# Kernel tuning notes

Measured on AMD Instinct MI355X. Metric: run time of the kernel, lower is better.

Reference implementation:

```python
import jax, jax.numpy as jnp
import numpy as np

SOS = 1  # from init_kwargs

def gru_cell(x, h, W_ih, W_hh, b_ih, b_hh):
    # torch nn.GRU single-step cell semantics
    gi = x @ W_ih.T + b_ih            # [B, 3H]
    gh = h @ W_hh.T + b_hh            # [B, 3H]
    i_r, i_z, i_n = jnp.split(gi, 3, axis=-1)
    h_r, h_z, h_n = jnp.split(gh, 3, axis=-1)
    r = jax.nn.sigmoid(i_r + h_r)
    z = jax.nn.sigmoid(i_z + h_z)
    n = jnp.tanh(i_n + r * h_n)
    return (1.0 - z) * n + z * h

def setup_inputs() -> dict:
    key = jax.random.key(0)
    ks = jax.random.split(key, 12)
    V, E, H, L, B = 32000, 512, 512, 2, 32
    s = lambda k, shape: (jax.random.normal(k, shape, jnp.float32) * 0.05)
    return dict(
        h_0=s(ks[0], (L, B, H)),
        emb=s(ks[1], (V, E)),
        W_ih0=s(ks[2], (3 * H, E)), W_hh0=s(ks[3], (3 * H, H)),
        b_ih0=s(ks[4], (3 * H,)),   b_hh0=s(ks[5], (3 * H,)),
        W_ih1=s(ks[6], (3 * H, H)), W_hh1=s(ks[7], (3 * H, H)),
        b_ih1=s(ks[8], (3 * H,)),   b_hh1=s(ks[9], (3 * H,)),
        W_out=s(ks[10], (V, H)),    b_out=s(ks[11], (V,)),
        max_n=64,
    )

def reference(h_0, emb, W_ih0, W_hh0, b_ih0, b_hh0,
              W_ih1, W_hh1, b_ih1, b_hh1, W_out, b_out, max_n):
    B = h_0.shape[1]
    tok0 = jnp.full((B,), SOS, dtype=jnp.int32)

    def step(carry, _):
        h, tok = carry                              # h: [2, B, H], tok: [B]
        x = emb[tok]                                # [B, E] embedding gather
        h0n = gru_cell(x,   h[0], W_ih0, W_hh0, b_ih0, b_hh0)
        h1n = gru_cell(h0n, h[1], W_ih1, W_hh1, b_ih1, b_hh1)
        logits = h1n @ W_out.T + b_out              # [B, V]
        ntok = jnp.argmax(logits, axis=-1).astype(jnp.int32)
        return (jnp.stack([h0n, h1n]), ntok), ntok

    (h_t, _), toks = jax.lax.scan(step, (h_0, tok0), None, length=max_n)
    # toks: [max_n, B] -> [B, max_n] to mirror per-sequence output lists
    return toks.T, h_t
```

## Files before the change

### kernel.cpp

```cpp
#include <hip/hip_runtime.h>
#include <math.h>

#define NBLK 256
#define NTHR 512
#define Bsz  32
#define Hsz  512
#define Vsz  32000
#define BH   (Bsz*Hsz)
#define LDP  516
#define CBLK 250
#define EPS  0.0045f

#define WS_HBUF   0
#define WS_PACKED 131072
#define WS_PLB    135168
#define WS_BAR    139264
#define WS_WPACK  143360
#define WS_WNORM  32911360
#define WS_CBAR   33039360
#define WS_NEEDED 33043456

#define PACKED_SEED 0x00000000FFFFFFFEull

typedef short short8 __attribute__((ext_vector_type(8)));
typedef float f32x4  __attribute__((ext_vector_type(4)));

struct Args {
  const float* h0_init;
  const float* emb;
  const float* Wih0; const float* Whh0; const float* bih0; const float* bhh0;
  const float* Wih1; const float* Whh1; const float* bih1; const float* bhh1;
  const float* Wout; const float* bout;
  const int*   maxn;
  float* out;
  float* hbuf;
  unsigned long long* packed;
  unsigned* plb;
  unsigned* bar;
  unsigned* cbar;
  const unsigned* wpack;
  const float* wnormE;
};

__device__ __forceinline__ unsigned short bf16_rne(float f){
  unsigned u = __float_as_uint(f);
  unsigned r = u + 0x7FFFu + ((u >> 16) & 1u);
  return (unsigned short)(r >> 16);
}
__device__ __forceinline__ float bf16v(float f){
  unsigned u = ((unsigned)bf16_rne(f)) << 16;
  return __uint_as_float(u);
}
__device__ __forceinline__ unsigned short bf16_ru(float f){
  unsigned u = __float_as_uint(f);
  unsigned t = u >> 16;
  if (!(u & 0x80000000u)) { if (u & 0xFFFFu) t++; }
  return (unsigned short)t;
}
__device__ __forceinline__ unsigned key32(float f){
  unsigned u = __float_as_uint(f);
  return (u & 0x80000000u) ? ~u : (u | 0x80000000u);
}

__device__ __forceinline__ unsigned long long cload8(const void* p){
  return __hip_atomic_load((const unsigned long long*)p,
                           __ATOMIC_RELAXED, __HIP_MEMORY_SCOPE_AGENT);
}
__device__ __forceinline__ unsigned cload4u(const unsigned* p){
  return __hip_atomic_load(p, __ATOMIC_RELAXED, __HIP_MEMORY_SCOPE_AGENT);
}
__device__ __forceinline__ void cstore4(float* p, float v){
  __hip_atomic_store(p, v, __ATOMIC_RELAXED, __HIP_MEMORY_SCOPE_AGENT);
}
__device__ __forceinline__ void cstore4u(unsigned* p, unsigned v){
  __hip_atomic_store(p, v, __ATOMIC_RELAXED, __HIP_MEMORY_SCOPE_AGENT);
}
__device__ __forceinline__ void cstore8(void* p, unsigned long long v){
  __hip_atomic_store((unsigned long long*)p, v,
                     __ATOMIC_RELAXED, __HIP_MEMORY_SCOPE_AGENT);
}

__device__ __forceinline__ short8 ntload8(const void* p){
  return __builtin_nontemporal_load((const short8*)p);
}

__device__ __forceinline__ void gridbar(unsigned* bar, int bid){
  __syncthreads();
  if (threadIdx.x == 0){
    asm volatile("s_waitcnt vmcnt(0)" ::: "memory");
    const int g = bid & 7;
    unsigned* gcnt = bar + g*32;
    unsigned* root = bar + 8*32;
    unsigned* gen  = bar + (9+g)*32;
    unsigned mygen = __hip_atomic_load(gen, __ATOMIC_RELAXED, __HIP_MEMORY_SCOPE_AGENT);
    unsigned go = __hip_atomic_fetch_add(gcnt, 1u, __ATOMIC_RELAXED, __HIP_MEMORY_SCOPE_AGENT);
    if (go == 31u){
      unsigned ro = __hip_atomic_fetch_add(root, 1u, __ATOMIC_RELAXED, __HIP_MEMORY_SCOPE_AGENT);
      if (ro == 7u){
        #pragma unroll
        for (int i = 0; i < 8; ++i)
          __hip_atomic_store(bar + i*32, 0u, __ATOMIC_RELAXED, __HIP_MEMORY_SCOPE_AGENT);
        __hip_atomic_store(root, 0u, __ATOMIC_RELAXED, __HIP_MEMORY_SCOPE_AGENT);
        asm volatile("s_waitcnt vmcnt(0)" ::: "memory");
        #pragma unroll
        for (int i = 0; i < 8; ++i)
          __hip_atomic_fetch_add(bar + (9+i)*32, 1u, __ATOMIC_RELAXED, __HIP_MEMORY_SCOPE_AGENT);
      }
    }
    while (__hip_atomic_load(gen, __ATOMIC_RELAXED, __HIP_MEMORY_SCOPE_AGENT) == mygen){
      __builtin_amdgcn_s_sleep(1);
    }
  }
  __syncthreads();
}

__device__ __forceinline__ void cluster_sync(unsigned* cnt, unsigned target){
  __syncthreads();
  if (threadIdx.x == 0){
    asm volatile("s_waitcnt vmcnt(0)" ::: "memory");
    __hip_atomic_fetch_add(cnt, 1u, __ATOMIC_RELAXED, __HIP_MEMORY_SCOPE_AGENT);
    while (__hip_atomic_load(cnt, __ATOMIC_RELAXED, __HIP_MEMORY_SCOPE_AGENT) < target){
      __builtin_amdgcn_s_sleep(1);
    }
  }
  __syncthreads();
}

__device__ __forceinline__ void stage_h(const float* g, float* s, int tid){
  const unsigned long long* gd = (const unsigned long long*)g;
  #pragma unroll
  for (int n = 0; n < 16; ++n){
    int idx = n*512 + tid;
    int row = idx >> 8;
    int col = idx & 255;
    unsigned long long v = __hip_atomic_load(gd + idx, __ATOMIC_RELAXED,
                                             __HIP_MEMORY_SCOPE_AGENT);
    *(unsigned long long*)(s + row*LDP + col*2) = v;
  }
}

__device__ __forceinline__ void stage_row(const float* g, float* s, int tid){
  if (tid < 256){
    unsigned long long v = __hip_atomic_load((const unsigned long long*)g + tid,
                                             __ATOMIC_RELAXED, __HIP_MEMORY_SCOPE_AGENT);
    *(unsigned long long*)(s + tid*2) = v;
  }
}

__device__ __forceinline__ float red8(float v){
  v += __shfl_xor(v, 1); v += __shfl_xor(v, 2); v += __shfl_xor(v, 4);
  return v;
}
__device__ __forceinline__ float dot4acc(float4 w, float4 x, float acc){
  return fmaf(w.x,x.x, fmaf(w.y,x.y, fmaf(w.z,x.z, fmaf(w.w,x.w, acc))));
}

__device__ __forceinline__ void dot3(const float* row, const float* W, int j,
                                     int lane8, float& g0, float& g1, float& g2){
  const float* w = W + (size_t)j * Hsz;
  float a0 = 0.f, a1 = 0.f, a2 = 0.f;
  #pragma unroll 4
  for (int i = 0; i < 16; ++i){
    int k = i*32 + lane8*4;
    float4 v = *(const float4*)(row + k);
    a0 = dot4acc(*(const float4*)(w + k),            v, a0);
    a1 = dot4acc(*(const float4*)(w + 512*512 + k),  v, a1);
    a2 = dot4acc(*(const float4*)(w + 2*512*512 + k),v, a2);
  }
  g0 = red8(a0); g1 = red8(a1); g2 = red8(a2);
}

__device__ __forceinline__ void gru_oct(
    const float* xrow, const float* hrow,
    const float* Wih, const float* Whh,
    const float* bih, const float* bhh,
    int j, int lane8, float* hout_g)
{
  const float* wir = Wih + (size_t)j * Hsz;
  const float* whr = Whh + (size_t)j * Hsz;
  float ar=0.f, az=0.f, an=0.f, hr=0.f, hz=0.f, hn=0.f;
  #pragma unroll 4
  for (int i = 0; i < 16; ++i){
    int k = i*32 + lane8*4;
    float4 xv = *(const float4*)(xrow + k);
    float4 hv = *(const float4*)(hrow + k);
    ar = dot4acc(*(const float4*)(wir + k),            xv, ar);
    az = dot4acc(*(const float4*)(wir + 512*512 + k),  xv, az);
    an = dot4acc(*(const float4*)(wir + 2*512*512 + k),xv, an);
    hr = dot4acc(*(const float4*)(whr + k),            hv, hr);
    hz = dot4acc(*(const float4*)(whr + 512*512 + k),  hv, hz);
    hn = dot4acc(*(const float4*)(whr + 2*512*512 + k),hv, hn);
  }
  ar = red8(ar); az = red8(az); an = red8(an);
  hr = red8(hr); hz = red8(hz); hn = red8(hn);
  if (lane8 == 0){
    float r = 1.f/(1.f + expf(-(ar + bih[j]       + hr + bhh[j])));
    float z = 1.f/(1.f + expf(-(az + bih[Hsz+j]   + hz + bhh[Hsz+j])));
    float n = tanhf(an + bih[2*Hsz+j] + r*(hn + bhh[2*Hsz+j]));
    cstore4(hout_g, (1.f - z)*n + z*hrow[j]);
  }
}

__global__ __launch_bounds__(512) void repack_kernel(const float* __restrict__ Wout,
                                                     unsigned* __restrict__ wpack,
                                                     float* __restrict__ wnormE){
  const int rb = blockIdx.x;
  const int g = threadIdx.x >> 6;
  const int lane = threadIdx.x & 63;
  const int n = rb*128 + g*16 + (lane & 15);
  const int kq = (lane >> 4) * 8;
  float sumsq = 0.f;
  for (int c = 0; c < 16; ++c){
    const float* p = Wout + (size_t)n*512 + c*32 + kq;
    float4 f0 = *(const float4*)p;
    float4 f1 = *(const float4*)(p + 4);
    unsigned short s0 = bf16_rne(f0.x), s1 = bf16_rne(f0.y),
                   s2 = bf16_rne(f0.z), s3 = bf16_rne(f0.w),
                   s4 = bf16_rne(f1.x), s5 = bf16_rne(f1.y),
                   s6 = bf16_rne(f1.z), s7 = bf16_rne(f1.w);
    float v;
    v = __uint_as_float(((unsigned)s0)<<16); sumsq += v*v;
    v = __uint_as_float(((unsigned)s1)<<16); sumsq += v*v;
    v = __uint_as_float(((unsigned)s2)<<16); sumsq += v*v;
    v = __uint_as_float(((unsigned)s3)<<16); sumsq += v*v;
    v = __uint_as_float(((unsigned)s4)<<16); sumsq += v*v;
    v = __uint_as_float(((unsigned)s5)<<16); sumsq += v*v;
    v = __uint_as_float(((unsigned)s6)<<16); sumsq += v*v;
    v = __uint_as_float(((unsigned)s7)<<16); sumsq += v*v;
    uint4 u;
    u.x = (unsigned)s0 | ((unsigned)s1<<16);
    u.y = (unsigned)s2 | ((unsigned)s3<<16);
    u.z = (unsigned)s4 | ((unsigned)s5<<16);
    u.w = (unsigned)s6 | ((unsigned)s7<<16);
    *(uint4*)(wpack + (size_t)(((rb*8+g)*16 + c))*256 + lane*4) = u;
  }
  sumsq += __shfl_xor(sumsq, 16);
  sumsq += __shfl_xor(sumsq, 32);
  if (lane < 16) wnormE[n] = EPS * sqrtf(sumsq);
}

__global__ __launch_bounds__(NTHR, 1) void decoder_kernel(Args a){
  const int tid = threadIdx.x;
  const int bid = blockIdx.x;
  const int wave = tid >> 6;
  const int lane = tid & 63;
  const int b  = bid >> 3;
  const int s  = bid & 7;
  const int j0 = s * 64;
  const int T = a.maxn[0];
  float* h0g = a.hbuf;
  float* h1g = a.hbuf + BH;

  __shared__ float shB[Bsz*LDP];
  __shared__ float h0row[LDP];
  __shared__ unsigned af[16*64*4];
  __shared__ unsigned long long ubq8[128*8];
  __shared__ float ghA[3][64];
  __shared__ float ghB[3][64];
  __shared__ float h0own[64];
  __shared__ float h1own[64];
  __shared__ unsigned lbmaxL[32];
  __shared__ unsigned maxlbL[32];
  __shared__ float hnormL[32];
  __shared__ int sh_tok0;
  __shared__ int candCnt;
  __shared__ int candList[512];
  unsigned short* ubq16 = (unsigned short*)ubq8;

  short8 bw[16];
  float bias = 0.f, wn = 0.f;
  if (bid < CBLK){
    const unsigned* wbase = a.wpack + (size_t)((bid*8 + wave)*16)*256 + lane*4;
    #pragma unroll
    for (int c = 0; c < 16; ++c){
      bw[c] = ntload8(wbase + c*256);
      asm volatile("" : "+a"(bw[c]));
    }
    int n = bid*128 + wave*16 + (lane & 15);
    bias = a.bout[n];
    wn = a.wnormE[n];
  }

  if (tid < 64){
    h0own[tid] = a.h0_init[(size_t)b*Hsz + j0 + tid];
    h1own[tid] = a.h0_init[BH + (size_t)b*Hsz + j0 + tid];
  }
  stage_row(a.h0_init + (size_t)b*Hsz, h0row, tid);
  stage_h(a.h0_init + BH, shB, tid);
  __syncthreads();
  {
    int oct = tid >> 3, lane8 = tid & 7;
    int j = j0 + oct;
    float hr, hz, hn;  dot3(h0row, a.Whh0, j, lane8, hr, hz, hn);
    float kr, kz, kn;  dot3(shB + b*LDP, a.Whh1, j, lane8, kr, kz, kn);
    if (lane8 == 0){
      ghA[0][oct] = hr; ghA[1][oct] = hz; ghA[2][oct] = hn;
      ghB[0][oct] = kr; ghB[1][oct] = kz; ghB[2][oct] = kn;
    }
  }
  __syncthreads();

  unsigned ctarget = 0;
  for (int t = 0; t < T; ++t){
    if (tid == 0){
      int tok = 1;
      if (t > 0){
        tok = (int)(~(unsigned)(cload8(&a.packed[b*16]) & 0xffffffffULL));
        if ((unsigned)tok >= (unsigned)Vsz) tok = 1;
      }
      sh_tok0 = tok;
    }
    __syncthreads();
    {
      int oct = tid >> 3, lane8 = tid & 7;
      int j = j0 + oct;
      const float* xrow = a.emb + (size_t)sh_tok0 * Hsz;
      float ar, az, an;  dot3(xrow, a.Wih0, j, lane8, ar, az, an);
      if (lane8 == 0){
        float hr = ghA[0][oct], hz = ghA[1][oct], hn = ghA[2][oct];
        float r = 1.f/(1.f + expf(-(ar + a.bih0[j]       + hr + a.bhh0[j])));
        float z = 1.f/(1.f + expf(-(az + a.bih0[Hsz+j]   + hz + a.bhh0[Hsz+j])));
        float n = tanhf(an + a.bih0[2*Hsz+j] + r*(hn + a.bhh0[2*Hsz+j]));
        float hnew = (1.f - z)*n + z*h0own[oct];
        cstore4(h0g + (size_t)b*Hsz + j, hnew);
        h0own[oct] = hnew;
      }
    }
    ctarget += 8;
    cluster_sync(a.cbar + b*32, ctarget);

    if (s == 0 && tid == 0){
      if (t > 0){
        unsigned long long p = cload8(&a.packed[b*16]);
        int tok = (int)(~(unsigned)(p & 0xffffffffULL));
        a.out[(size_t)b*T + (t-1)] = (float)tok;
      }
      cstore8(&a.packed[b*16], PACKED_SEED);
      cstore4u(&a.plb[b*32], 0u);
    }
    stage_row(h0g + (size_t)b*Hsz, h0row, tid);
    __syncthreads();
    {
      int oct = tid >> 3, lane8 = tid & 7;
      int j = j0 + oct;
      float ar, az, an;  dot3(h0row, a.Wih1, j, lane8, ar, az, an);
      if (lane8 == 0){
        float hr = ghB[0][oct], hz = ghB[1][oct], hn = ghB[2][oct];
        float r = 1.f/(1.f + expf(-(ar + a.bih1[j]       + hr + a.bhh1[j])));
        float z = 1.f/(1.f + expf(-(az + a.bih1[Hsz+j]   + hz + a.bhh1[Hsz+j])));
        float n = tanhf(an + a.bih1[2*Hsz+j] + r*(hn + a.bhh1[2*Hsz+j]));
        float hnew = (1.f - z)*n + z*h1own[oct];
        cstore4(h1g + (size_t)b*Hsz + j, hnew);
        h1own[oct] = hnew;
      }
    }
    gridbar(a.bar, bid);

    stage_h(h1g, shB, tid);
    if (tid < 32) lbmaxL[tid] = 0u;
    if (tid == 0) candCnt = 0;
    __syncthreads();
    {
      int oct = tid >> 3, lane8 = tid & 7;
      int j = j0 + oct;
      float hr, hz, hn;  dot3(h0row, a.Whh0, j, lane8, hr, hz, hn);
      float kr, kz, kn;  dot3(shB + b*LDP, a.Whh1, j, lane8, kr, kz, kn);
      if (lane8 == 0){
        ghA[0][oct] = hr; ghA[1][oct] = hz; ghA[2][oct] = hn;
        ghB[0][oct] = kr; ghB[1][oct] = kz; ghB[2][oct] = kn;
      }
    }
    if (bid < CBLK){
      #pragma unroll
      for (int c = 0; c < 16; ++c) asm volatile("" : "+a"(bw[c]));

      if (tid < 256){
        int hb = tid >> 3, lane8 = tid & 7;
        float sq = 0.f;
        #pragma unroll
        for (int i = 0; i < 8; ++i){
          const float* p = shB + hb*LDP + i*64 + lane8*8;
          #pragma unroll
          for (int q = 0; q < 8; ++q){ float v = bf16v(p[q]); sq = fmaf(v, v, sq); }
        }
        sq = red8(sq);
        if (lane8 == 0) hnormL[hb] = sqrtf(sq);
      }

      f32x4 accs[2];
      #pragma unroll
      for (int mt = 0; mt < 2; ++mt){
        #pragma unroll
        for (int it = 0; it < 8; ++it){
          int d = it*512 + tid;
          int c = d >> 8, al = (d >> 2) & 63, dw = d & 3;
          int m = mt*16 + (al & 15);
          int k = c*32 + ((al >> 4) * 8) + dw*2;
          unsigned lo = bf16_rne(shB[m*LDP + k]);
          unsigned hi = bf16_rne(shB[m*LDP + k + 1]);
          af[d] = lo | (hi << 16);
        }
        __syncthreads();
        f32x4 acc = {0.f, 0.f, 0.f, 0.f};
        #pragma unroll
        for (int c = 0; c < 16; ++c){
          short8 av = *(short8*)&af[(c*64 + lane)*4];
          acc = __builtin_amdgcn_mfma_f32_16x16x32_bf16(av, bw[c], acc, 0, 0, 0);
        }
        accs[mt] = acc;
        __syncthreads();
      }
      {
        int n_loc = wave*16 + (lane & 15);
        int quad = lane >> 4;
        #pragma unroll
        for (int mt = 0; mt < 2; ++mt){
          unsigned long long pk = 0ULL;
          #pragma unroll
          for (int r = 0; r < 4; ++r){
            int m = mt*16 + quad*4 + r;
            float lg = accs[mt][r] + bias;
            float mg = wn * hnormL[m];
            float lb = lg - mg;
            float ub = lg + mg;
            pk |= ((unsigned long long)bf16_ru(ub)) << (16*r);
            unsigned lk = key32(lb), o;
            o = __shfl_xor(lk, 1); lk = lk > o ? lk : o;
            o = __shfl_xor(lk, 2); lk = lk > o ? lk : o;
            o = __shfl_xor(lk, 4); lk = lk > o ? lk : o;
            o = __shfl_xor(lk, 8); lk = lk > o ? lk : o;
            if ((lane & 15) == 0) atomicMax(&lbmaxL[m], lk);
          }
          ubq8[n_loc*8 + mt*4 + quad] = pk;
        }
      }
      __syncthreads();
      if (tid < 32) atomicMax(&a.plb[tid*32], lbmaxL[tid]);
      for (int u = 0; u < 8; ++u){
        int idx = u*512 + tid;
        unsigned short q = ubq16[idx];
        float uf = __uint_as_float(((unsigned)q) << 16);
        if (key32(uf) >= lbmaxL[idx & 31]){
          int pos = atomicAdd(&candCnt, 1);
          if (pos < 512) candList[pos] = idx;
        }
      }
      __syncthreads();
      if (tid < 32){
        unsigned g = cload4u(&a.plb[tid*32]);
        unsigned l = lbmaxL[tid];
        maxlbL[tid] = g > l ? g : l;
      }
      __syncthreads();
      auto rescore = [&](int cidx){
        int n_loc = cidx >> 5, rb = cidx & 31;
        unsigned short q = ubq16[cidx];
        float uf = __uint_as_float(((unsigned)q) << 16);
        if (key32(uf) < maxlbL[rb]) return;
        int n = bid*128 + n_loc;
        const float* wrow = a.Wout + (size_t)n*512 + lane*8;
        const float* hrow = shB + rb*LDP + lane*8;
        float4 w0 = *(const float4*)wrow,      w1 = *(const float4*)(wrow + 4);
        float4 x0 = *(const float4*)hrow,      x1 = *(const float4*)(hrow + 4);
        float d = dot4acc(w0, x0, 0.f);
        d = dot4acc(w1, x1, d);
        d += __shfl_xor(d, 1);  d += __shfl_xor(d, 2);  d += __shfl_xor(d, 4);
        d += __shfl_xor(d, 8);  d += __shfl_xor(d, 16); d += __shfl_xor(d, 32);
        if (lane == 0){
          float lg = d + a.bout[n];
          unsigned long long key =
              (((unsigned long long)key32(lg)) << 32) | (unsigned)(~(unsigned)n);
          atomicMax(&a.packed[rb*16], key);
        }
      };
      int nc = candCnt;
      if (nc <= 512){
        for (int ci = wave; ci < nc; ci += 8) rescore(candList[ci]);
      } else {
        for (int ci = wave; ci < 4096; ci += 8) rescore(ci);
      }
    }
    gridbar(a.bar, bid);
  }

  if (bid == 0 && tid < Bsz){
    unsigned long long p = cload8(&a.packed[tid*16]);
    int tok = (int)(~(unsigned)(p & 0xffffffffULL));
    a.out[tid*T + (T-1)] = (float)tok;
  }
  int e = bid*NTHR + tid;
  if (e < BH/2){
    unsigned long long v0 = cload8((const unsigned long long*)h0g + e);
    unsigned long long v1 = cload8((const unsigned long long*)h1g + e);
    *((unsigned long long*)(a.out + Bsz*T) + e)      = v0;
    *((unsigned long long*)(a.out + Bsz*T + BH) + e) = v1;
  }
}

__global__ __launch_bounds__(NTHR, 1) void decoder_kernel_fb(Args a){
  const int tid = threadIdx.x;
  const int bid = blockIdx.x;
  const int T = a.maxn[0];
  float* h0g = a.hbuf;
  float* h1g = a.hbuf + BH;
  __shared__ float shA[Bsz*LDP];
  __shared__ float shB[Bsz*LDP];
  __shared__ unsigned long long lbest[32*32];
  __shared__ int sh_tok[Bsz];

  for (int t = 0; t < T; ++t){
    if (t == 0) stage_h(a.h0_init, shA, tid);
    if (tid < Bsz){
      int tok;
      if (t == 0) tok = 1;
      else {
        tok = (int)(~(unsigned)(cload8(&a.packed[tid*16]) & 0xffffffffULL));
        if ((unsigned)tok >= (unsigned)Vsz) tok = 1;
      }
      sh_tok[tid] = tok;
    }
    __syncthreads();
    {
      int oct = tid >> 3, lane8 = tid & 7;
      int b = oct & 31, jj = oct >> 5;
      int j = bid*2 + jj;
      const float* xrow = a.emb + (size_t)sh_tok[b] * Hsz;
      gru_oct(xrow, shA + b*LDP, a.Wih0, a.Whh0, a.bih0, a.bhh0,
              j, lane8, h0g + b*Hsz + j);
    }
    gridbar(a.bar, bid);
    if (bid == 0 && tid < Bsz){
      if (t > 0){
        unsigned long long p = cload8(&a.packed[tid*16]);
        a.out[tid*T + (t-1)] = (float)((int)(~(unsigned)(p & 0xffffffffULL)));
      }
      cstore8(&a.packed[tid*16], PACKED_SEED);
    }
    stage_h(h0g, shA, tid);
    if (t == 0) stage_h(a.h0_init + BH, shB, tid);
    __syncthreads();
    {
      int oct = tid >> 3, lane8 = tid & 7;
      int b = oct & 31, jj = oct >> 5;
      int j = bid*2 + jj;
      gru_oct(shA + b*LDP, shB + b*LDP, a.Wih1, a.Whh1, a.bih1, a.bhh1,
              j, lane8, h1g + b*Hsz + j);
    }
    gridbar(a.bar, bid);
    stage_h(h1g, shB, tid);
    __syncthreads();
    if (bid < CBLK){
      const int quad = tid >> 2, l4 = tid & 3;
      const int rg = quad & 31, bg = quad >> 5;
      const int rowbase = bid*128 + rg*4;
      const float* wr = a.Wout + (size_t)rowbase * Hsz;
      const float* hb = shB + bg*8*LDP;
      float acc[4][8];
      #pragma unroll
      for (int s = 0; s < 4; ++s)
        #pragma unroll
        for (int j = 0; j < 8; ++j) acc[s][j] = 0.f;
      #pragma unroll 2
      for (int i = 0; i < 32; ++i){
        const int k = i*16 + l4*4;
        float4 wv[4], hv[8];
        #pragma unroll
        for (int s = 0; s < 4; ++s) wv[s] = *(const float4*)(wr + (size_t)s*Hsz + k);
        #pragma unroll
        for (int j = 0; j < 8; ++j) hv[j] = *(const float4*)(hb + j*LDP + k);
        #pragma unroll
        for (int s = 0; s < 4; ++s)
          #pragma unroll
          for (int j = 0; j < 8; ++j) acc[s][j] = dot4acc(wv[s], hv[j], acc[s][j]);
      }
      #pragma unroll
      for (int s = 0; s < 4; ++s)
        #pragma unroll
        for (int j = 0; j < 8; ++j){
          float v = acc[s][j];
          v += __shfl_xor(v, 1); v += __shfl_xor(v, 2);
          acc[s][j] = v;
        }
      if (l4 == 0){
        float4 bv = *(const float4*)(a.bout + rowbase);
        float bb[4] = {bv.x, bv.y, bv.z, bv.w};
        #pragma unroll
        for (int j = 0; j < 8; ++j){
          float best = -3.4e38f; int bi = rowbase;
          #pragma unroll
          for (int s = 0; s < 4; ++s){
            float lv = acc[s][j] + bb[s];
            if (lv > best){ best = lv; bi = rowbase + s; }
          }
          unsigned u = __float_as_uint(best);
          unsigned key = (u & 0x80000000u) ? ~u : (u | 0x80000000u);
          lbest[rg*32 + bg*8 + j] =
              ((unsigned long long)key << 32) | (unsigned)(~(unsigned)bi);
        }
      }
      __syncthreads();
      if (tid < Bsz){
        unsigned long long m = lbest[tid];
        #pragma unroll 4
        for (int r = 1; r < 32; ++r){
          unsigned long long c = lbest[r*32 + tid];
          m = (c > m) ? c : m;
        }
        atomicMax(&a.packed[tid*16], m);
      }
    }
    gridbar(a.bar, bid);
  }
  if (bid == 0 && tid < Bsz){
    unsigned long long p = cload8(&a.packed[tid*16]);
    a.out[tid*T + (T-1)] = (float)((int)(~(unsigned)(p & 0xffffffffULL)));
  }
  int e = bid*NTHR + tid;
  if (e < BH/2){
    unsigned long long v0 = cload8((const unsigned long long*)h0g + e);
    unsigned long long v1 = cload8((const unsigned long long*)h1g + e);
    *((unsigned long long*)(a.out + Bsz*T) + e)      = v0;
    *((unsigned long long*)(a.out + Bsz*T + BH) + e) = v1;
  }
}

extern "C" void kernel_launch(void* const* d_in, const int* in_sizes, int n_in,
                              void* d_out, int out_size, void* d_ws, size_t ws_size,
                              hipStream_t stream){
  Args a;
  a.h0_init = (const float*)d_in[0];
  a.emb  = (const float*)d_in[1];
  a.Wih0 = (const float*)d_in[2];
  a.Whh0 = (const float*)d_in[3];
  a.bih0 = (const float*)d_in[4];
  a.bhh0 = (const float*)d_in[5];
  a.Wih1 = (const float*)d_in[6];
  a.Whh1 = (const float*)d_in[7];
  a.bih1 = (const float*)d_in[8];
  a.bhh1 = (const float*)d_in[9];
  a.Wout = (const float*)d_in[10];
  a.bout = (const float*)d_in[11];
  a.maxn = (const int*)d_in[12];
  a.out  = (float*)d_out;
  char* wsb = (char*)d_ws;
  a.hbuf   = (float*)(wsb + WS_HBUF);
  a.packed = (unsigned long long*)(wsb + WS_PACKED);
  a.plb    = (unsigned*)(wsb + WS_PLB);
  a.bar    = (unsigned*)(wsb + WS_BAR);
  a.cbar   = (unsigned*)(wsb + WS_CBAR);
  a.wpack  = (const unsigned*)(wsb + WS_WPACK);
  a.wnormE = (const float*)(wsb + WS_WNORM);

  hipMemsetAsync(wsb + WS_PACKED, 0, 12288, stream);

  void* params[] = { &a };
  if (ws_size >= (size_t)WS_NEEDED){
    hipMemsetAsync(wsb + WS_CBAR, 0, 4096, stream);
    repack_kernel<<<CBLK, 512, 0, stream>>>(a.Wout, (unsigned*)a.wpack, (float*)a.wnormE);
    hipLaunchCooperativeKernel((void*)decoder_kernel, dim3(NBLK), dim3(NTHR),
                               params, 0, stream);
  } else {
    hipLaunchCooperativeKernel((void*)decoder_kernel_fb, dim3(NBLK), dim3(NTHR),
                               params, 0, stream);
  }
}
```

Baseline: 2.636 ms.

## Stage layer-1 hidden state directly as bf16 and feed MFMA from row layout

The full layer-1 hidden state is now staged into shared memory as bf16 instead of fp32, converted while loading. MFMA A-operands are read directly from this row-major bf16 tile, which removes the separate repack pass into a fragment buffer and two block barriers per tile. The GRU recurrence now uses a separate fp32 row for its own batch element. Candidate rescoring loads the fp32 hidden row from global memory instead of shared, so that rescore adds global traffic in exchange for lower shared-memory use and shorter staging.

```diff
diff --git a/kernel.cpp b/kernel.cpp
--- a/kernel.cpp
+++ b/kernel.cpp
@@ -8,6 +8,7 @@
 #define Vsz  32000
 #define BH   (Bsz*Hsz)
 #define LDP  516
+#define LDPB 520
 #define CBLK 250
 #define EPS  0.0045f
 
@@ -124,6 +125,21 @@
     }
   }
   __syncthreads();
+}
+
+__device__ __forceinline__ void stage_h16(const float* g, unsigned short* s16, int tid){
+  const unsigned long long* gd = (const unsigned long long*)g;
+  #pragma unroll
+  for (int n = 0; n < 16; ++n){
+    int idx = n*512 + tid;
+    int row = idx >> 8;
+    int col2 = idx & 255;
+    unsigned long long v = __hip_atomic_load(gd + idx, __ATOMIC_RELAXED,
+                                             __HIP_MEMORY_SCOPE_AGENT);
+    unsigned short b0 = bf16_rne(__uint_as_float((unsigned)v));
+    unsigned short b1 = bf16_rne(__uint_as_float((unsigned)(v >> 32)));
+    *(unsigned*)&s16[row*LDPB + col2*2] = (unsigned)b0 | ((unsigned)b1 << 16);
+  }
 }
 
 __device__ __forceinline__ void stage_h(const float* g, float* s, int tid){
@@ -251,9 +267,9 @@
   float* h0g = a.hbuf;
   float* h1g = a.hbuf + BH;
 
-  __shared__ float shB[Bsz*LDP];
+  __shared__ __align__(16) unsigned short shB16[Bsz*LDPB];
   __shared__ float h0row[LDP];
-  __shared__ unsigned af[16*64*4];
+  __shared__ float h1row[LDP];
   __shared__ unsigned long long ubq8[128*8];
   __shared__ float ghA[3][64];
   __shared__ float ghB[3][64];
@@ -286,13 +302,13 @@
     h1own[tid] = a.h0_init[BH + (size_t)b*Hsz + j0 + tid];
   }
   stage_row(a.h0_init + (size_t)b*Hsz, h0row, tid);
-  stage_h(a.h0_init + BH, shB, tid);
+  stage_row(a.h0_init + BH + (size_t)b*Hsz, h1row, tid);
   __syncthreads();
   {
     int oct = tid >> 3, lane8 = tid & 7;
     int j = j0 + oct;
     float hr, hz, hn;  dot3(h0row, a.Whh0, j, lane8, hr, hz, hn);
-    float kr, kz, kn;  dot3(shB + b*LDP, a.Whh1, j, lane8, kr, kz, kn);
+    float kr, kz, kn;  dot3(h1row, a.Whh1, j, lane8, kr, kz, kn);
     if (lane8 == 0){
       ghA[0][oct] = hr; ghA[1][oct] = hz; ghA[2][oct] = hn;
       ghB[0][oct] = kr; ghB[1][oct] = kz; ghB[2][oct] = kn;
@@ -356,7 +372,8 @@
     }
     gridbar(a.bar, bid);
 
-    stage_h(h1g, shB, tid);
+    if (bid < CBLK) stage_h16(h1g, shB16, tid);
+    stage_row(h1g + (size_t)b*Hsz, h1row, tid);
     if (tid < 32) lbmaxL[tid] = 0u;
     if (tid == 0) candCnt = 0;
     __syncthreads();
@@ -364,7 +381,7 @@
       int oct = tid >> 3, lane8 = tid & 7;
       int j = j0 + oct;
       float hr, hz, hn;  dot3(h0row, a.Whh0, j, lane8, hr, hz, hn);
-      float kr, kz, kn;  dot3(shB + b*LDP, a.Whh1, j, lane8, kr, kz, kn);
+      float kr, kz, kn;  dot3(h1row, a.Whh1, j, lane8, kr, kz, kn);
       if (lane8 == 0){
         ghA[0][oct] = hr; ghA[1][oct] = hz; ghA[2][oct] = hn;
         ghB[0][oct] = kr; ghB[1][oct] = kz; ghB[2][oct] = kn;
@@ -379,9 +396,12 @@
         float sq = 0.f;
         #pragma unroll
         for (int i = 0; i < 8; ++i){
-          const float* p = shB + hb*LDP + i*64 + lane8*8;
+          short8 sv = *(const short8*)&shB16[hb*LDPB + i*64 + lane8*8];
           #pragma unroll
-          for (int q = 0; q < 8; ++q){ float v = bf16v(p[q]); sq = fmaf(v, v, sq); }
+          for (int q = 0; q < 8; ++q){
+            float v = __uint_as_float(((unsigned)(unsigned short)sv[q]) << 16);
+            sq = fmaf(v, v, sq);
+          }
         }
         sq = red8(sq);
         if (lane8 == 0) hnormL[hb] = sqrtf(sq);
@@ -390,26 +410,16 @@
       f32x4 accs[2];
       #pragma unroll
       for (int mt = 0; mt < 2; ++mt){
-        #pragma unroll
-        for (int it = 0; it < 8; ++it){
-          int d = it*512 + tid;
-          int c = d >> 8, al = (d >> 2) & 63, dw = d & 3;
-          int m = mt*16 + (al & 15);
-          int k = c*32 + ((al >> 4) * 8) + dw*2;
-          unsigned lo = bf16_rne(shB[m*LDP + k]);
-          unsigned hi = bf16_rne(shB[m*LDP + k + 1]);
-          af[d] = lo | (hi << 16);
-        }
-        __syncthreads();
         f32x4 acc = {0.f, 0.f, 0.f, 0.f};
+        const unsigned short* arow = shB16 + (mt*16 + (lane & 15))*LDPB + (lane >> 4)*8;
         #pragma unroll
         for (int c = 0; c < 16; ++c){
-          short8 av = *(short8*)&af[(c*64 + lane)*4];
+          short8 av = *(const short8*)(arow + c*32);
           acc = __builtin_amdgcn_mfma_f32_16x16x32_bf16(av, bw[c], acc, 0, 0, 0);
         }
         accs[mt] = acc;
-        __syncthreads();
-      }
+      }
+      __syncthreads();
       {
         int n_loc = wave*16 + (lane & 15);
         int quad = lane >> 4;
@@ -459,9 +469,19 @@
         if (key32(uf) < maxlbL[rb]) return;
         int n = bid*128 + n_loc;
         const float* wrow = a.Wout + (size_t)n*512 + lane*8;
-        const float* hrow = shB + rb*LDP + lane*8;
+        const unsigned long long* hq =
+            (const unsigned long long*)(h1g + (size_t)rb*Hsz) + lane*4;
+        unsigned long long q0 = cload8(hq),     q1 = cload8(hq + 1);
+        unsigned long long q2 = cload8(hq + 2), q3 = cload8(hq + 3);
+        float4 x0 = make_float4(__uint_as_float((unsigned)q0),
+                                __uint_as_float((unsigned)(q0 >> 32)),
+                                __uint_as_float((unsigned)q1),
+                                __uint_as_float((unsigned)(q1 >> 32)));
+        float4 x1 = make_float4(__uint_as_float((unsigned)q2),
+                                __uint_as_float((unsigned)(q2 >> 32)),
+                                __uint_as_float((unsigned)q3),
+                                __uint_as_float((unsigned)(q3 >> 32)));
         float4 w0 = *(const float4*)wrow,      w1 = *(const float4*)(wrow + 4);
-        float4 x0 = *(const float4*)hrow,      x1 = *(const float4*)(hrow + 4);
         float d = dot4acc(w0, x0, 0.f);
         d = dot4acc(w1, x1, d);
         d += __shfl_xor(d, 1);  d += __shfl_xor(d, 2);  d += __shfl_xor(d, 4);
```

After: 2.676 ms. Within noise of the previous version (+1.5%).
